# Kernel tuning notes

Hardware: AMD Instinct MI355X
Metric: run time of the kernel (lower is better)

The kernel has to match this reference:

```python
import jax, jax.numpy as jnp
import numpy as np

S0, S1 = 256, 256          # spins (up, down)
N = S0 + S1                # total electrons
SINGLE = 256               # single_dim == single_out (residual requires match)
PAIR = 128                 # pair_dim == pair_out
GAIN_TANH = 1.5927812698663017  # ActivationWithGain: 1/std(tanh(N(0,1)))
SQRT2 = 1.4142135623730951


def setup_inputs() -> dict:
    key = jax.random.key(0)
    ks = jax.random.split(key, 7)
    h_one = jax.random.normal(ks[0], (N, SINGLE), jnp.float32)
    h_two = jax.random.normal(ks[1], (N, N, PAIR), jnp.float32)
    din = SINGLE + 2 * PAIR  # one_in feature dim = 512
    # variance_scaling(2, fan_in) kernels; bias ~ Normal(0, sqrt(2))
    W1 = jax.random.normal(ks[2], (din, SINGLE), jnp.float32) * (2.0 / din) ** 0.5
    b1 = jax.random.normal(ks[3], (SINGLE,), jnp.float32) * SQRT2
    Wg = jax.random.normal(ks[4], (2 * SINGLE, SINGLE), jnp.float32) * (2.0 / (2 * SINGLE)) ** 0.5
    W2 = jax.random.normal(ks[5], (PAIR, PAIR), jnp.float32) * (2.0 / PAIR) ** 0.5
    b2 = jax.random.normal(ks[6], (PAIR,), jnp.float32) * SQRT2
    return dict(h_one=h_one, h_two=h_two, W1=W1, b1=b1, Wg=Wg, W2=W2, b2=b2)


def _act(x):
    # ActivationWithGain(tanh): rescale so output variance ~ input variance
    return jnp.tanh(x) * jnp.asarray(GAIN_TANH, x.dtype)


def reference(h_one, h_two, W1, b1, Wg, W2, b2):
    # construct_single_features: per-spin mean of h_two over sender axis
    g2_up = jnp.mean(h_two[:S0], axis=0)            # (N, PAIR)
    g2_dn = jnp.mean(h_two[S0:], axis=0)            # (N, PAIR)
    one_in = jnp.concatenate([h_one, g2_up, g2_dn], axis=1)   # (N, SINGLE+2*PAIR)
    # construct_global_features: per-spin mean of h_one, concat on features
    g1_up = jnp.mean(h_one[:S0], axis=0, keepdims=True)       # (1, SINGLE)
    g1_dn = jnp.mean(h_one[S0:], axis=0, keepdims=True)       # (1, SINGLE)
    global_in = jnp.concatenate([g1_up, g1_dn], axis=-1)      # (1, 2*SINGLE)

    h_one_new = one_in @ W1 + b1 + global_in @ Wg             # (N, SINGLE)
    h_one_new = _act(h_one_new / SQRT2)
    h_one_out = (h_one + h_one_new) / SQRT2                   # residual (shapes match)

    h_two_new = _act(h_two @ W2 + b2)                         # (N, N, PAIR)
    h_two_out = (h_two + h_two_new) / SQRT2                   # residual
    return h_one_out, h_two_out
```

## Files before the change

### kernel.cpp

```cpp
#include <hip/hip_runtime.h>
#include <stdint.h>

#define NN 512
#define PAIR 128
#define SINGLE 256

#define GAINv 1.5927812698663017f
#define RS2 0.70710678118654752f

typedef unsigned int uint;
typedef unsigned short ushort;
typedef short bf16x8 __attribute__((ext_vector_type(8)));
typedef float f32x4 __attribute__((ext_vector_type(4)));

__device__ __forceinline__ ushort f2b(float f){
  union{float f;uint i;}v; v.f=f;
  uint x=v.i;
  return (ushort)((x + 0x7FFFu + ((x>>16)&1u))>>16);
}
__device__ __forceinline__ float b2f(ushort u){ union{uint i;float f;}v; v.i=((uint)u)<<16; return v.f; }
__device__ __forceinline__ float b2f_lo(uint u){ union{uint i;float f;}v; v.i=u<<16; return v.f; }
__device__ __forceinline__ float b2f_hi(uint u){ union{uint i;float f;}v; v.i=u&0xFFFF0000u; return v.f; }
__device__ __forceinline__ float tanh_fast(float x){
  float xc = fminf(fmaxf(x,-8.f),8.f);
  float e = __expf(2.f*xc);
  return (e-1.f)*__builtin_amdgcn_rcpf(e+1.f);
}
__device__ __forceinline__ void gload_lds16(const void* g, void* lds){
  __builtin_amdgcn_global_load_lds(
      (const __attribute__((address_space(1))) uint32_t*)g,
      (__attribute__((address_space(3))) uint32_t*)lds, 16, 0, 0);
}

__global__ __launch_bounds__(256) void k1_prep(const float* __restrict__ h_one,
                                               const float* __restrict__ w2,
                                               float* __restrict__ g1acc,
                                               ushort* __restrict__ wt)
{
  const int b = blockIdx.x, t = threadIdx.x;
  if(b < 8){
    const int rb = b*64;
    float s = 0.f;
    for(int i=0;i<64;i++) s += h_one[(size_t)(rb+i)*SINGLE + t];
    atomicAdd(&g1acc[(b>>2)*SINGLE + t], s);
  } else {
    const int bb = b-8;
    for(int e=t; e<16*128; e+=256){
      int kl = e>>7, n = e&127;
      int k = bb*16 + kl;
      wt[n*128 + k] = f2b(w2[(size_t)k*128 + n]);
    }
  }
}

__global__ __launch_bounds__(256) void k2_gterm(const float* __restrict__ g1acc,
                                                const float* __restrict__ wg,
                                                float* __restrict__ gterm)
{
  const int t = threadIdx.x;
  const int fb = blockIdx.x*64;
  float s = 0.f;
  for(int f=fb; f<fb+64; f++)
    s += g1acc[f]*(1.f/256.f)*wg[(size_t)f*SINGLE + t];
  atomicAdd(&gterm[t], s);
}

__global__ __launch_bounds__(256, 2) void k3_htwo(
    const float* __restrict__ h_two,
    const float* __restrict__ b2,
    const ushort* __restrict__ wt,
    float* __restrict__ g2acc,
    float* __restrict__ out_h2)
{
  __shared__ __align__(16) ushort At[128*128];
  __shared__ __align__(16) ushort Wt[128*128];
  const int tid  = threadIdx.x;
  const int wave = tid>>6, lane = tid&63;
  const int bi = blockIdx.x & 15, bj = blockIdx.x >> 4;
  const int i0 = bi*32, j0 = bj*4;

  for(int t=0;t<8;t++){
    int q = wave*8+t;
    gload_lds16(wt + q*512 + lane*8, &Wt[q*512]);
  }
  #pragma unroll
  for(int rep=0; rep<16; rep++){
    int e = rep*1024 + tid*4;
    int di = e>>9, c = e&511;
    float4 v = *(const float4*)(h_two + ((size_t)(i0+di)*NN + j0)*PAIR + c);
    ushort4 pk; pk.x=f2b(v.x); pk.y=f2b(v.y); pk.z=f2b(v.z); pk.w=f2b(v.w);
    *(ushort4*)(&At[e]) = pk;
  }
  __syncthreads();

  {
    const int dj = tid>>6, pp = tid&63;
    const uint* a32 = (const uint*)At;
    float s0=0.f, s1=0.f;
    #pragma unroll
    for(int di=0;di<32;di++){
      uint u = a32[(di*4+dj)*64 + pp];
      s0 += b2f_lo(u); s1 += b2f_hi(u);
    }
    const int spin = bi>>3;
    float* dst = g2acc + ((size_t)spin*NN + (j0+dj))*PAIR + pp*2;
    atomicAdd(dst, s0); atomicAdd(dst+1, s1);
  }

  const int wm = wave&1, wn = wave>>1;
  const int lq = lane>>4, lr = lane&15;
  f32x4 acc[4][4];
  #pragma unroll
  for(int a=0;a<4;a++)
    #pragma unroll
    for(int b=0;b<4;b++) acc[a][b]=(f32x4){0.f,0.f,0.f,0.f};

  #pragma unroll
  for(int kk=0;kk<4;kk++){
    const int k0 = kk*32 + lq*8;
    bf16x8 af[4], bfr[4];
    #pragma unroll
    for(int nt=0;nt<4;nt++){
      int n = wn*64 + nt*16 + lr;
      af[nt] = *(const bf16x8*)(&Wt[n*128 + k0]);
    }
    #pragma unroll
    for(int mt=0;mt<4;mt++){
      int m = wm*64 + mt*16 + lr;
      bfr[mt] = *(const bf16x8*)(&At[m*128 + k0]);
    }
    #pragma unroll
    for(int mt=0;mt<4;mt++)
      #pragma unroll
      for(int nt=0;nt<4;nt++)
        acc[mt][nt] = __builtin_amdgcn_mfma_f32_16x16x32_bf16(af[nt], bfr[mt], acc[mt][nt], 0,0,0);
  }

  #pragma unroll
  for(int mt=0;mt<4;mt++){
    const int m = wm*64 + mt*16 + lr;
    const size_t base = ((size_t)(i0 + (m>>2))*NN + (j0 + (m&3)))*PAIR;
    #pragma unroll
    for(int nt=0;nt<4;nt++){
      const int nb = wn*64 + nt*16 + lq*4;
      float4 bb = *(const float4*)(b2 + nb);
      float4 rr = *(const float4*)(h_two + base + nb);
      float4 o;
      o.x = (rr.x + GAINv*tanh_fast(acc[mt][nt][0] + bb.x))*RS2;
      o.y = (rr.y + GAINv*tanh_fast(acc[mt][nt][1] + bb.y))*RS2;
      o.z = (rr.z + GAINv*tanh_fast(acc[mt][nt][2] + bb.z))*RS2;
      o.w = (rr.w + GAINv*tanh_fast(acc[mt][nt][3] + bb.w))*RS2;
      *(float4*)(out_h2 + base + nb) = o;
    }
  }
}

__global__ __launch_bounds__(256) void k4_hone(
    const float* __restrict__ h_one,
    const float* __restrict__ w1,
    const float* __restrict__ b1,
    const float* __restrict__ g2acc,
    const float* __restrict__ gterm,
    float* __restrict__ out_h1)
{
  __shared__ float onein[512];
  const int n   = threadIdx.x;
  const int row = blockIdx.x;
  onein[n] = h_one[(size_t)row*SINGLE + n];
  {
    int spin = n>>7, p = n&127;
    onein[256 + n] = g2acc[((size_t)spin*NN + row)*PAIR + p] * (1.f/256.f);
  }
  __syncthreads();
  float acc = 0.f;
  for(int f=0; f<512; f++)
    acc += onein[f] * w1[(size_t)f*SINGLE + n];
  float x = (acc + b1[n] + gterm[n]) * RS2;
  float o = (onein[n] + GAINv*tanh_fast(x)) * RS2;
  out_h1[(size_t)row*SINGLE + n] = o;
}

extern "C" void kernel_launch(void* const* d_in, const int* in_sizes, int n_in,
                              void* d_out, int out_size, void* d_ws, size_t ws_size,
                              hipStream_t stream)
{
  const float* h_one = (const float*)d_in[0];
  const float* h_two = (const float*)d_in[1];
  const float* W1    = (const float*)d_in[2];
  const float* b1    = (const float*)d_in[3];
  const float* Wg    = (const float*)d_in[4];
  const float* W2    = (const float*)d_in[5];
  const float* b2    = (const float*)d_in[6];

  float* wsf    = (float*)d_ws;
  float* g2acc  = wsf;
  float* g1acc  = wsf + 131072;
  float* gterm  = wsf + 131584;
  ushort* wt    = (ushort*)(wsf + 131840);

  float* out_h1 = (float*)d_out;
  float* out_h2 = out_h1 + 131072;

  hipMemsetAsync(wsf, 0, (size_t)(131072+512+256)*sizeof(float), stream);
  k1_prep <<<16,   256, 0, stream>>>(h_one, W2, g1acc, wt);
  k2_gterm<<<8,    256, 0, stream>>>(g1acc, Wg, gterm);
  k3_htwo <<<2048, 256, 0, stream>>>(h_two, b2, wt, g2acc, out_h2);
  k4_hone <<<512,  256, 0, stream>>>(h_one, W1, b1, g2acc, gterm, out_h1);
}
```

Measured before the change: 306.5 us.

## Restructure h_two kernel to register-resident streaming per column, drop atomics and memset

The main h_two kernel is rewritten. Each block now owns one receiver column j for one spin, keeps W2 fragments in registers and streams 16 chunks of 16 sender rows straight from global memory into MFMA operands, with no LDS staging. The per-spin mean is reduced in registers with wave shuffles and written once, so the global atomics and the hipMemset go away; the g1 and gterm paths become partial-sum buffers. The k4 kernel handles two rows per block to reuse W1 loads. The risks are lower memory-level parallelism per wave, uncoalesced strided row access, and the loss of LDS reuse of h_two, which is now read twice (operand and residual).

```diff
diff --git a/kernel.cpp b/kernel.cpp
--- a/kernel.cpp
+++ b/kernel.cpp
@@ -18,23 +18,15 @@
   uint x=v.i;
   return (ushort)((x + 0x7FFFu + ((x>>16)&1u))>>16);
 }
-__device__ __forceinline__ float b2f(ushort u){ union{uint i;float f;}v; v.i=((uint)u)<<16; return v.f; }
-__device__ __forceinline__ float b2f_lo(uint u){ union{uint i;float f;}v; v.i=u<<16; return v.f; }
-__device__ __forceinline__ float b2f_hi(uint u){ union{uint i;float f;}v; v.i=u&0xFFFF0000u; return v.f; }
 __device__ __forceinline__ float tanh_fast(float x){
   float xc = fminf(fmaxf(x,-8.f),8.f);
   float e = __expf(2.f*xc);
   return (e-1.f)*__builtin_amdgcn_rcpf(e+1.f);
 }
-__device__ __forceinline__ void gload_lds16(const void* g, void* lds){
-  __builtin_amdgcn_global_load_lds(
-      (const __attribute__((address_space(1))) uint32_t*)g,
-      (__attribute__((address_space(3))) uint32_t*)lds, 16, 0, 0);
-}
 
 __global__ __launch_bounds__(256) void k1_prep(const float* __restrict__ h_one,
                                                const float* __restrict__ w2,
-                                               float* __restrict__ g1acc,
+                                               float* __restrict__ g1part,
                                                ushort* __restrict__ wt)
 {
   const int b = blockIdx.x, t = threadIdx.x;
@@ -42,7 +34,7 @@
     const int rb = b*64;
     float s = 0.f;
     for(int i=0;i<64;i++) s += h_one[(size_t)(rb+i)*SINGLE + t];
-    atomicAdd(&g1acc[(b>>2)*SINGLE + t], s);
+    g1part[b*SINGLE + t] = s;
   } else {
     const int bb = b-8;
     for(int e=t; e<16*128; e+=256){
@@ -53,105 +45,110 @@
   }
 }
 
-__global__ __launch_bounds__(256) void k2_gterm(const float* __restrict__ g1acc,
+__global__ __launch_bounds__(256) void k2_gterm(const float* __restrict__ g1part,
                                                 const float* __restrict__ wg,
-                                                float* __restrict__ gterm)
-{
+                                                float* __restrict__ gtermpart)
+{
+  __shared__ float g1m[512];
   const int t = threadIdx.x;
+  g1m[t]     = (g1part[t]      + g1part[256+t]  + g1part[512+t]  + g1part[768+t])  * (1.f/256.f);
+  g1m[t+256] = (g1part[1024+t] + g1part[1280+t] + g1part[1536+t] + g1part[1792+t]) * (1.f/256.f);
+  __syncthreads();
   const int fb = blockIdx.x*64;
   float s = 0.f;
   for(int f=fb; f<fb+64; f++)
-    s += g1acc[f]*(1.f/256.f)*wg[(size_t)f*SINGLE + t];
-  atomicAdd(&gterm[t], s);
-}
-
-__global__ __launch_bounds__(256, 2) void k3_htwo(
+    s += g1m[f]*wg[(size_t)f*SINGLE + t];
+  gtermpart[blockIdx.x*SINGLE + t] = s;
+}
+
+__global__ __launch_bounds__(256, 3) void k3_htwo(
     const float* __restrict__ h_two,
     const float* __restrict__ b2,
     const ushort* __restrict__ wt,
     float* __restrict__ g2acc,
     float* __restrict__ out_h2)
 {
-  __shared__ __align__(16) ushort At[128*128];
-  __shared__ __align__(16) ushort Wt[128*128];
   const int tid  = threadIdx.x;
-  const int wave = tid>>6, lane = tid&63;
-  const int bi = blockIdx.x & 15, bj = blockIdx.x >> 4;
-  const int i0 = bi*32, j0 = bj*4;
-
-  for(int t=0;t<8;t++){
-    int q = wave*8+t;
-    gload_lds16(wt + q*512 + lane*8, &Wt[q*512]);
-  }
-  #pragma unroll
-  for(int rep=0; rep<16; rep++){
-    int e = rep*1024 + tid*4;
-    int di = e>>9, c = e&511;
-    float4 v = *(const float4*)(h_two + ((size_t)(i0+di)*NN + j0)*PAIR + c);
-    ushort4 pk; pk.x=f2b(v.x); pk.y=f2b(v.y); pk.z=f2b(v.z); pk.w=f2b(v.w);
-    *(ushort4*)(&At[e]) = pk;
-  }
-  __syncthreads();
-
-  {
-    const int dj = tid>>6, pp = tid&63;
-    const uint* a32 = (const uint*)At;
-    float s0=0.f, s1=0.f;
-    #pragma unroll
-    for(int di=0;di<32;di++){
-      uint u = a32[(di*4+dj)*64 + pp];
-      s0 += b2f_lo(u); s1 += b2f_hi(u);
-    }
-    const int spin = bi>>3;
-    float* dst = g2acc + ((size_t)spin*NN + (j0+dj))*PAIR + pp*2;
-    atomicAdd(dst, s0); atomicAdd(dst+1, s1);
-  }
-
-  const int wm = wave&1, wn = wave>>1;
-  const int lq = lane>>4, lr = lane&15;
-  f32x4 acc[4][4];
-  #pragma unroll
-  for(int a=0;a<4;a++)
-    #pragma unroll
-    for(int b=0;b<4;b++) acc[a][b]=(f32x4){0.f,0.f,0.f,0.f};
-
-  #pragma unroll
-  for(int kk=0;kk<4;kk++){
-    const int k0 = kk*32 + lq*8;
-    bf16x8 af[4], bfr[4];
-    #pragma unroll
-    for(int nt=0;nt<4;nt++){
-      int n = wn*64 + nt*16 + lr;
-      af[nt] = *(const bf16x8*)(&Wt[n*128 + k0]);
-    }
-    #pragma unroll
-    for(int mt=0;mt<4;mt++){
-      int m = wm*64 + mt*16 + lr;
-      bfr[mt] = *(const bf16x8*)(&At[m*128 + k0]);
-    }
-    #pragma unroll
-    for(int mt=0;mt<4;mt++)
+  const int w    = tid>>6, lane = tid&63;
+  const int lq   = lane>>4, lr = lane&15;
+  const int spin = blockIdx.x >> 9;
+  const int j    = blockIdx.x & 511;
+
+  bf16x8 af[2][4];
+  #pragma unroll
+  for(int nt=0;nt<2;nt++){
+    const int n = w*32 + nt*16 + lr;
+    #pragma unroll
+    for(int s=0;s<4;s++){
+      const int q = (s + w) & 3;
+      af[nt][s] = *(const bf16x8*)(wt + n*128 + q*32 + lq*8);
+    }
+  }
+  f32x4 bias[2];
+  #pragma unroll
+  for(int nt=0;nt<2;nt++){
+    const float4 bv = *(const float4*)(b2 + w*32 + nt*16 + lq*4);
+    bias[nt] = (f32x4){bv.x, bv.y, bv.z, bv.w};
+  }
+
+  const size_t row0 = (size_t)spin*256 + lr;
+  const float* rp = h_two + (row0*NN + j)*PAIR;
+  float*       op = out_h2 + (row0*NN + j)*PAIR;
+  const size_t cstep = (size_t)16*NN*PAIR;
+
+  float g2r[8] = {0.f,0.f,0.f,0.f,0.f,0.f,0.f,0.f};
+
+  #pragma unroll 1
+  for(int c=0;c<16;c++){
+    const float* rb = rp + (size_t)c*cstep;
+    float4 S[8];
+    #pragma unroll
+    for(int s=0;s<4;s++){
+      const int q = (s + w) & 3;
+      S[s*2]   = *(const float4*)(rb + q*32 + lq*8);
+      S[s*2+1] = *(const float4*)(rb + q*32 + lq*8 + 4);
+    }
+    const float4 R0 = *(const float4*)(rb + w*32 + lq*4);
+    const float4 R1 = *(const float4*)(rb + w*32 + 16 + lq*4);
+
+    g2r[0]+=S[0].x; g2r[1]+=S[0].y; g2r[2]+=S[0].z; g2r[3]+=S[0].w;
+    g2r[4]+=S[1].x; g2r[5]+=S[1].y; g2r[6]+=S[1].z; g2r[7]+=S[1].w;
+
+    f32x4 acc0 = bias[0], acc1 = bias[1];
+    #pragma unroll
+    for(int s=0;s<4;s++){
+      bf16x8 bfr;
+      const float* sv = (const float*)&S[s*2];
       #pragma unroll
-      for(int nt=0;nt<4;nt++)
-        acc[mt][nt] = __builtin_amdgcn_mfma_f32_16x16x32_bf16(af[nt], bfr[mt], acc[mt][nt], 0,0,0);
-  }
-
-  #pragma unroll
-  for(int mt=0;mt<4;mt++){
-    const int m = wm*64 + mt*16 + lr;
-    const size_t base = ((size_t)(i0 + (m>>2))*NN + (j0 + (m&3)))*PAIR;
-    #pragma unroll
-    for(int nt=0;nt<4;nt++){
-      const int nb = wn*64 + nt*16 + lq*4;
-      float4 bb = *(const float4*)(b2 + nb);
-      float4 rr = *(const float4*)(h_two + base + nb);
-      float4 o;
-      o.x = (rr.x + GAINv*tanh_fast(acc[mt][nt][0] + bb.x))*RS2;
-      o.y = (rr.y + GAINv*tanh_fast(acc[mt][nt][1] + bb.y))*RS2;
-      o.z = (rr.z + GAINv*tanh_fast(acc[mt][nt][2] + bb.z))*RS2;
-      o.w = (rr.w + GAINv*tanh_fast(acc[mt][nt][3] + bb.w))*RS2;
-      *(float4*)(out_h2 + base + nb) = o;
-    }
+      for(int e=0;e<8;e++) bfr[e] = (short)f2b(sv[e]);
+      acc0 = __builtin_amdgcn_mfma_f32_16x16x32_bf16(af[0][s], bfr, acc0, 0,0,0);
+      acc1 = __builtin_amdgcn_mfma_f32_16x16x32_bf16(af[1][s], bfr, acc1, 0,0,0);
+    }
+
+    float* ob = op + (size_t)c*cstep + w*32 + lq*4;
+    f32x4 o0, o1;
+    o0[0] = (R0.x + GAINv*tanh_fast(acc0[0]))*RS2;
+    o0[1] = (R0.y + GAINv*tanh_fast(acc0[1]))*RS2;
+    o0[2] = (R0.z + GAINv*tanh_fast(acc0[2]))*RS2;
+    o0[3] = (R0.w + GAINv*tanh_fast(acc0[3]))*RS2;
+    o1[0] = (R1.x + GAINv*tanh_fast(acc1[0]))*RS2;
+    o1[1] = (R1.y + GAINv*tanh_fast(acc1[1]))*RS2;
+    o1[2] = (R1.z + GAINv*tanh_fast(acc1[2]))*RS2;
+    o1[3] = (R1.w + GAINv*tanh_fast(acc1[3]))*RS2;
+    __builtin_nontemporal_store(o0, (f32x4*)ob);
+    __builtin_nontemporal_store(o1, (f32x4*)(ob+16));
+  }
+
+  #pragma unroll
+  for(int m=1;m<16;m<<=1){
+    #pragma unroll
+    for(int q=0;q<8;q++) g2r[q] += __shfl_xor(g2r[q], m, 64);
+  }
+  if(lr < 2){
+    f32x4 v;
+    if(lr==0){ v[0]=g2r[0]; v[1]=g2r[1]; v[2]=g2r[2]; v[3]=g2r[3]; }
+    else     { v[0]=g2r[4]; v[1]=g2r[5]; v[2]=g2r[6]; v[3]=g2r[7]; }
+    *(f32x4*)(g2acc + ((size_t)spin*NN + j)*PAIR + w*32 + lq*8 + lr*4) = v;
   }
 }
 
@@ -160,24 +157,33 @@
     const float* __restrict__ w1,
     const float* __restrict__ b1,
     const float* __restrict__ g2acc,
-    const float* __restrict__ gterm,
+    const float* __restrict__ gtermpart,
     float* __restrict__ out_h1)
 {
-  __shared__ float onein[512];
-  const int n   = threadIdx.x;
-  const int row = blockIdx.x;
-  onein[n] = h_one[(size_t)row*SINGLE + n];
-  {
-    int spin = n>>7, p = n&127;
-    onein[256 + n] = g2acc[((size_t)spin*NN + row)*PAIR + p] * (1.f/256.f);
-  }
+  __shared__ float onein[2][512];
+  const int n  = threadIdx.x;
+  const int r0 = blockIdx.x*2;
+  #pragma unroll
+  for(int rr=0; rr<2; rr++){
+    onein[rr][n] = h_one[(size_t)(r0+rr)*SINGLE + n];
+    int sp = n>>7, p = n&127;
+    onein[rr][256+n] = g2acc[((size_t)sp*NN + (r0+rr))*PAIR + p] * (1.f/256.f);
+  }
+  float gt = 0.f;
+  #pragma unroll
+  for(int bb=0;bb<8;bb++) gt += gtermpart[bb*256+n];
   __syncthreads();
-  float acc = 0.f;
-  for(int f=0; f<512; f++)
-    acc += onein[f] * w1[(size_t)f*SINGLE + n];
-  float x = (acc + b1[n] + gterm[n]) * RS2;
-  float o = (onein[n] + GAINv*tanh_fast(x)) * RS2;
-  out_h1[(size_t)row*SINGLE + n] = o;
+  float a0=0.f, a1=0.f;
+  for(int f=0; f<512; f++){
+    float wv = w1[(size_t)f*SINGLE + n];
+    a0 += onein[0][f]*wv;
+    a1 += onein[1][f]*wv;
+  }
+  const float bn = b1[n];
+  float x0 = (a0 + bn + gt)*RS2;
+  float x1 = (a1 + bn + gt)*RS2;
+  out_h1[(size_t)r0*SINGLE + n]     = (onein[0][n] + GAINv*tanh_fast(x0))*RS2;
+  out_h1[(size_t)(r0+1)*SINGLE + n] = (onein[1][n] + GAINv*tanh_fast(x1))*RS2;
 }
 
 extern "C" void kernel_launch(void* const* d_in, const int* in_sizes, int n_in,
@@ -192,18 +198,17 @@
   const float* W2    = (const float*)d_in[5];
   const float* b2    = (const float*)d_in[6];
 
-  float* wsf    = (float*)d_ws;
-  float* g2acc  = wsf;
-  float* g1acc  = wsf + 131072;
-  float* gterm  = wsf + 131584;
-  ushort* wt    = (ushort*)(wsf + 131840);
+  float* wsf       = (float*)d_ws;
+  float* g2acc     = wsf;
+  ushort* wt       = (ushort*)(wsf + 131072);
+  float* g1part    = wsf + 139264;
+  float* gtermpart = wsf + 141312;
 
   float* out_h1 = (float*)d_out;
   float* out_h2 = out_h1 + 131072;
 
-  hipMemsetAsync(wsf, 0, (size_t)(131072+512+256)*sizeof(float), stream);
-  k1_prep <<<16,   256, 0, stream>>>(h_one, W2, g1acc, wt);
-  k2_gterm<<<8,    256, 0, stream>>>(g1acc, Wg, gterm);
-  k3_htwo <<<2048, 256, 0, stream>>>(h_two, b2, wt, g2acc, out_h2);
-  k4_hone <<<512,  256, 0, stream>>>(h_one, W1, b1, g2acc, gterm, out_h1);
-}
+  k1_prep <<<16,   256, 0, stream>>>(h_one, W2, g1part, wt);
+  k2_gterm<<<8,    256, 0, stream>>>(g1part, Wg, gtermpart);
+  k3_htwo <<<1024, 256, 0, stream>>>(h_two, b2, wt, g2acc, out_h2);
+  k4_hone <<<256,  256, 0, stream>>>(h_one, W1, b1, g2acc, gtermpart, out_h1);
+}
```

After: 340.0 us. 11.0% more time.
